# Kernel optimization log

Measured on AMD Instinct MI355X. Metric: run time of the kernel, lower is better.

The kernel has to match this reference:

```python
import jax, jax.numpy as jnp
import numpy as np

B, L, D, Y = 8, 2500, 512, 8921

def setup_inputs() -> dict:
    key = jax.random.key(0)
    k1, k2, k3, k4 = jax.random.split(key, 4)
    x = jax.random.normal(k1, (B, L, D), dtype=jnp.float32)
    # xavier-ish init scale for the label-attention and output matrices
    scale = (2.0 / (Y + D)) ** 0.5
    U_w = jax.random.normal(k2, (Y, D), dtype=jnp.float32) * scale
    final_w = jax.random.normal(k3, (Y, D), dtype=jnp.float32) * scale
    final_b = jax.random.normal(k4, (Y,), dtype=jnp.float32) * 0.01
    return {"x": x, "U_w": U_w, "final_w": final_w, "final_b": final_b}

def reference(x, U_w, final_w, final_b):
    # scores[b, y, l] = U_w[y, :] . x[b, l, :]
    scores = jnp.einsum('yd,bld->byl', U_w, x)            # (B, Y, L)
    alpha = jax.nn.softmax(scores, axis=2)                 # softmax over seq dim
    m = jnp.einsum('byl,bld->byd', alpha, x)               # (B, Y, D)
    y = jnp.einsum('yd,byd->by', final_w, m) + final_b     # (B, Y)
    return y
```

## Files before the change

kernel.cpp:

```cpp
#include <hip/hip_runtime.h>
#include <hip/hip_bf16.h>

#define NB 8
#define NL 2500
#define ND 512
#define NY 8921

#define BM 256
#define BN 256
#define BK 32
#define NKS 16
#define LPAD 2560
#define NLT 10
#define NYB 70
#define YPAD 8960

#define SPLIT 5
#define LSPL_MAIN 2

#define TILE 16384
#define GT_BYTES ((size_t)NYB * NKS * TILE)
#define XT_BYTES ((size_t)NB * NLT * NKS * TILE)
#define P_ELEMS  ((size_t)SPLIT * NB * YPAD)
#define P_BYTES  (P_ELEMS * 4)

typedef short s8v __attribute__((ext_vector_type(8)));
typedef float f4v __attribute__((ext_vector_type(4)));

__device__ __forceinline__ unsigned short f2bf(float f) {
  unsigned int u = __float_as_uint(f);
  return (unsigned short)((u + 0x7FFFu + ((u >> 16) & 1u)) >> 16);
}
__device__ __forceinline__ unsigned int pk2(float a, float b) {
  return (unsigned int)f2bf(a) | ((unsigned int)f2bf(b) << 16);
}
__device__ __forceinline__ void async_copy16(const char* g, char* l) {
  __builtin_amdgcn_global_load_lds(
      (const __attribute__((address_space(1))) void*)g,
      (__attribute__((address_space(3))) void*)l, 16, 0, 0);
}

__device__ __forceinline__ int tile_off(int r, int gn) {
  int rp = r >> 1;
  return rp * 128 + ((((r & 1) << 6) | (gn << 4)) ^ ((rp & 7) << 4));
}

__global__ void cvt_g_kernel(const float* __restrict__ U, const float* __restrict__ W,
                             char* __restrict__ Gt) {
  int c = blockIdx.x * 256 + threadIdx.x;
  int g10 = c & 1023;
  int tile = c >> 10;
  int ks = tile & 15, yblk = tile >> 4;
  int r = g10 >> 2, gn = g10 & 3;
  int rg = yblk * 256 + r;
  int y = rg >> 1;
  uint4 o;
  if (y < NY) {
    const float* src = (rg & 1) ? W : U;
    const float4* p = (const float4*)(src + (size_t)y * ND + ks * BK + gn * 8);
    float4 f0 = p[0], f1 = p[1];
    o.x = pk2(f0.x, f0.y); o.y = pk2(f0.z, f0.w);
    o.z = pk2(f1.x, f1.y); o.w = pk2(f1.z, f1.w);
  } else {
    o = make_uint4(0u, 0u, 0u, 0u);
  }
  *(uint4*)(Gt + (size_t)tile * TILE + tile_off(r, gn)) = o;
}

__global__ void cvt_x_kernel(const float* __restrict__ x, char* __restrict__ Xt) {
  int c = blockIdx.x * 256 + threadIdx.x;
  int g10 = c & 1023;
  int tile = c >> 10;
  int ks = tile & 15, rest = tile >> 4;
  int t = rest % NLT, b = rest / NLT;
  int r = g10 >> 2, gn = g10 & 3;
  int l = t * 256 + r;
  uint4 o;
  if (l < NL) {
    const float4* p = (const float4*)(x + ((size_t)b * NL + l) * ND + ks * BK + gn * 8);
    float4 f0 = p[0], f1 = p[1];
    o.x = pk2(f0.x, f0.y); o.y = pk2(f0.z, f0.w);
    o.z = pk2(f1.x, f1.y); o.w = pk2(f1.z, f1.w);
  } else {
    o = make_uint4(0u, 0u, 0u, 0u);
  }
  *(uint4*)(Xt + (size_t)tile * TILE + tile_off(r, gn)) = o;
}

template<int LSPL, int NSPL, bool PARTIAL>
__global__ __launch_bounds__(512, 2) void fused_kernel(
    const char* __restrict__ Gt, const char* __restrict__ Xt,
    const float* __restrict__ bias, float* __restrict__ out,
    float* __restrict__ PD, float* __restrict__ PN)
{
  __shared__ uint4 ring[8192];
  char* ringC = (char*)ring;

  constexpr int NKT = LSPL * 8;

  const int tid  = threadIdx.x;
  const int lane = tid & 63;
  const int w    = tid >> 6;
  const int wr   = w >> 2;
  const int wc   = w & 3;
  const int cl   = lane & 15, g = lane >> 4;

  const int id    = blockIdx.x;
  const int bb    = id & 7;
  const int n     = id >> 3;
  const int yblk  = n / NSPL;
  const int split = n - yblk * NSPL;
  const int tbase = split * LSPL;

  const char* GA = Gt + (size_t)yblk * NKS * TILE;
  const char* XB = Xt + ((size_t)bb * NLT + tbase) * NKS * TILE;

  f4v acc[8][4];
  float runD[8][2], runN[8][2];
  #pragma unroll
  for (int mi = 0; mi < 8; ++mi)
    #pragma unroll
    for (int p = 0; p < 2; ++p) { runD[mi][p] = 0.f; runN[mi][p] = 0.f; }

  int aoff[8], boff[4];
  #pragma unroll
  for (int j = 0; j < 8; ++j) aoff[j] = tile_off(wr * 128 + j * 16 + cl, g);
  #pragma unroll
  for (int ni = 0; ni < 4; ++ni) boff[ni] = tile_off(wc * 64 + ni * 16 + cl, g);

  const int t16 = tid << 4;
  auto stgA = [&](int kt1, int par) {
    const char* ga = GA + (size_t)((((kt1 & 7) << 1) | par)) * TILE;
    char* la = ringC + (kt1 & 1) * 32768 + par * 16384 + (w << 10);
    async_copy16(ga + t16, la);
    async_copy16(ga + 8192 + t16, la + 8192);
  };
  auto stgB = [&](int kt1, int par) {
    const char* gb = XB + (size_t)((kt1 >> 3) * 16 + ((kt1 & 7) << 1) + par) * TILE;
    char* lb = ringC + 65536 + (kt1 & 1) * 32768 + par * 16384 + (w << 10);
    async_copy16(gb + t16, lb);
    async_copy16(gb + 8192 + t16, lb + 8192);
  };

  auto softmax_acc = [&](int tt) {
    const int lbase = (tbase + tt) * BN + wc * 64 + cl;
    #pragma unroll
    for (int mi = 0; mi < 8; ++mi) {
      #pragma unroll
      for (int p = 0; p < 2; ++p) {
        float se = 0.f, ste = 0.f;
        #pragma unroll
        for (int ni = 0; ni < 4; ++ni) {
          bool valid = (lbase + ni * 16) < NL;
          float sv = valid ? acc[mi][ni][2 * p] : -1e30f;
          float e = __expf(sv);
          se += e;
          ste += e * acc[mi][ni][2 * p + 1];
        }
        runD[mi][p] += se;
        runN[mi][p] += ste;
      }
    }
  };

#define SBAR __builtin_amdgcn_sched_barrier(0)
#define LGKM(N) asm volatile("s_waitcnt lgkmcnt(" #N ")" ::: "memory")
#define VMC(N)  asm volatile("s_waitcnt vmcnt(" #N ")" ::: "memory")

  stgA(0, 0); stgB(0, 0); stgA(0, 1); stgB(0, 1);
  VMC(4);
  __builtin_amdgcn_s_barrier();
  asm volatile("" ::: "memory");

  s8v bvE[4], bvO[4], afX[4], afY[4];
  #pragma unroll
  for (int ni = 0; ni < 4; ++ni) bvE[ni] = *(const s8v*)(ringC + 65536 + boff[ni]);
  #pragma unroll
  for (int j = 0; j < 4; ++j)    afX[j] = *(const s8v*)(ringC + aoff[j]);

  for (int kt = 0; kt < NKT; ++kt) {
    const int buf = kt & 1;
    const char* Ae = ringC + buf * 32768;
    const char* Ao = Ae + 16384;
    const char* Bo = ringC + 65536 + buf * 32768 + 16384;
    const char* Aen = ringC + (buf ^ 1) * 32768;
    const char* Ben = ringC + 65536 + (buf ^ 1) * 32768;
    const bool hn = (kt + 1) < NKT;

    if ((kt & 7) == 0) {
      if (kt > 0) softmax_acc((kt >> 3) - 1);
      #pragma unroll
      for (int mi = 0; mi < 8; ++mi)
        #pragma unroll
        for (int ni = 0; ni < 4; ++ni)
          #pragma unroll
          for (int q = 0; q < 4; ++q) acc[mi][ni][q] = 0.f;
    }

    if (hn) stgA(kt + 1, 0);
    #pragma unroll
    for (int j = 0; j < 4; ++j) afY[j] = *(const s8v*)(Ae + aoff[4 + j]);
    SBAR;
    __builtin_amdgcn_s_barrier();
    LGKM(4); SBAR;
    __builtin_amdgcn_s_setprio(1);
    #pragma unroll
    for (int j = 0; j < 4; ++j)
      #pragma unroll
      for (int ni = 0; ni < 4; ++ni)
        acc[j][ni] = __builtin_amdgcn_mfma_f32_16x16x32_bf16(afX[j], bvE[ni], acc[j][ni], 0, 0, 0);
    __builtin_amdgcn_s_setprio(0);
    if (hn) { VMC(2); } else { VMC(0); }
    SBAR;
    __builtin_amdgcn_s_barrier();
    asm volatile("" ::: "memory");

    if (hn) stgB(kt + 1, 0);
    #pragma unroll
    for (int ni = 0; ni < 4; ++ni) bvO[ni] = *(const s8v*)(Bo + boff[ni]);
    #pragma unroll
    for (int j = 0; j < 4; ++j)    afX[j] = *(const s8v*)(Ao + aoff[j]);
    SBAR;
    __builtin_amdgcn_s_barrier();
    LGKM(8); SBAR;
    __builtin_amdgcn_s_setprio(1);
    #pragma unroll
    for (int j = 0; j < 4; ++j)
      #pragma unroll
      for (int ni = 0; ni < 4; ++ni)
        acc[4 + j][ni] = __builtin_amdgcn_mfma_f32_16x16x32_bf16(afY[j], bvE[ni], acc[4 + j][ni], 0, 0, 0);
    __builtin_amdgcn_s_setprio(0);
    SBAR;
    __builtin_amdgcn_s_barrier();
    asm volatile("" ::: "memory");

    if (hn) stgA(kt + 1, 1);
    #pragma unroll
    for (int j = 0; j < 4; ++j) afY[j] = *(const s8v*)(Ao + aoff[4 + j]);
    SBAR;
    __builtin_amdgcn_s_barrier();
    LGKM(4); SBAR;
    __builtin_amdgcn_s_setprio(1);
    #pragma unroll
    for (int j = 0; j < 4; ++j)
      #pragma unroll
      for (int ni = 0; ni < 4; ++ni)
        acc[j][ni] = __builtin_amdgcn_mfma_f32_16x16x32_bf16(afX[j], bvO[ni], acc[j][ni], 0, 0, 0);
    __builtin_amdgcn_s_setprio(0);
    if (hn) VMC(2);
    SBAR;
    __builtin_amdgcn_s_barrier();
    asm volatile("" ::: "memory");

    if (hn) {
      stgB(kt + 1, 1);
      #pragma unroll
      for (int ni = 0; ni < 4; ++ni) bvE[ni] = *(const s8v*)(Ben + boff[ni]);
      #pragma unroll
      for (int j = 0; j < 4; ++j)    afX[j] = *(const s8v*)(Aen + aoff[j]);
      SBAR;
      __builtin_amdgcn_s_barrier();
      LGKM(8); SBAR;
    } else {
      SBAR;
      __builtin_amdgcn_s_barrier();
      LGKM(0); SBAR;
    }
    __builtin_amdgcn_s_setprio(1);
    #pragma unroll
    for (int j = 0; j < 4; ++j)
      #pragma unroll
      for (int ni = 0; ni < 4; ++ni)
        acc[4 + j][ni] = __builtin_amdgcn_mfma_f32_16x16x32_bf16(afY[j], bvO[ni], acc[4 + j][ni], 0, 0, 0);
    __builtin_amdgcn_s_setprio(0);
    SBAR;
    __builtin_amdgcn_s_barrier();
    asm volatile("" ::: "memory");
  }
  softmax_acc(LSPL - 1);

#undef SBAR
#undef LGKM
#undef VMC

  #pragma unroll
  for (int mi = 0; mi < 8; ++mi)
    #pragma unroll
    for (int p = 0; p < 2; ++p) {
      float d = runD[mi][p], nn = runN[mi][p];
      #pragma unroll
      for (int off = 1; off < 16; off <<= 1) {
        d += __shfl_xor(d, off);
        nn += __shfl_xor(nn, off);
      }
      runD[mi][p] = d; runN[mi][p] = nn;
    }

  __syncthreads();
  float* sm = (float*)ring;
  if (cl == 0) {
    #pragma unroll
    for (int mi = 0; mi < 8; ++mi)
      #pragma unroll
      for (int p = 0; p < 2; ++p) {
        int lab = wr * 64 + mi * 8 + 2 * g + p;
        float* s2 = sm + (lab * 4 + wc) * 2;
        s2[0] = runD[mi][p]; s2[1] = runN[mi][p];
      }
  }
  __syncthreads();
  if (tid < 128) {
    float D = 0.f, N = 0.f;
    #pragma unroll
    for (int q = 0; q < 4; ++q) {
      const float* s2 = sm + (tid * 4 + q) * 2;
      D += s2[0]; N += s2[1];
    }
    int y = yblk * 128 + tid;
    if constexpr (PARTIAL) {
      size_t o = ((size_t)split * NB + bb) * YPAD + y;
      PD[o] = D; PN[o] = N;
    } else {
      if (y < NY) out[(size_t)bb * NY + y] = N / D + bias[y];
    }
  }
}

__global__ void merge_kernel(const float* __restrict__ PD, const float* __restrict__ PN,
                             const float* __restrict__ bias, float* __restrict__ out) {
  int idx = blockIdx.x * 256 + threadIdx.x;
  int b = idx / YPAD, y = idx - b * YPAD;
  if (y >= NY) return;
  float D = 0.f, N = 0.f;
  #pragma unroll
  for (int s = 0; s < SPLIT; ++s) {
    size_t o = ((size_t)s * NB + b) * YPAD + y;
    D += PD[o];
    N += PN[o];
  }
  out[(size_t)b * NY + y] = N / D + bias[y];
}

extern "C" void kernel_launch(void* const* d_in, const int* in_sizes, int n_in,
                              void* d_out, int out_size, void* d_ws, size_t ws_size,
                              hipStream_t stream) {
  const float* xf   = (const float*)d_in[0];
  const float* Uf   = (const float*)d_in[1];
  const float* Wf   = (const float*)d_in[2];
  const float* bias = (const float*)d_in[3];
  float* out = (float*)d_out;

  char* Gt = (char*)d_ws;
  char* Xt = Gt + GT_BYTES;
  float* PD = (float*)(Xt + XT_BYTES);
  float* PN = PD + P_ELEMS;

  cvt_g_kernel<<<4480, 256, 0, stream>>>(Uf, Wf, Gt);
  cvt_x_kernel<<<5120, 256, 0, stream>>>(xf, Xt);

  const size_t need_main = GT_BYTES + XT_BYTES + 2 * P_BYTES;
  if (ws_size >= need_main) {
    fused_kernel<LSPL_MAIN, SPLIT, true><<<NYB * NB * SPLIT, 512, 0, stream>>>(
        Gt, Xt, bias, out, PD, PN);
    merge_kernel<<<NB * YPAD / 256, 256, 0, stream>>>(PD, PN, bias, out);
  } else {
    fused_kernel<NLT, 1, false><<<NYB * NB, 512, 0, stream>>>(
        Gt, Xt, bias, out, PD, PN);
  }
}
```

Measured before the change: 361.6 us.

## Switch GEMM from 16x16x32 to 32x32x16 MFMA with new warp tiling

Replaces the 16x16x32 bf16 MFMA with the larger 32x32x16 instruction and remaps the 8 waves from a 2x4 to a 4x2 grid, each computing 64x128 instead of 128x64. Fragment loads, LDS offsets, the softmax accumulation, the cross-lane reductions and the label index mapping are all rewritten for the 32x32 accumulator layout. The aim is to cut LDS fragment traffic per MFMA and raise per-instruction throughput. In exchange the output-row mapping becomes more intricate, which risks correctness errors, and the LDS read pattern changes, which may add bank conflicts.

```diff
diff --git a/kernel.cpp b/kernel.cpp
--- a/kernel.cpp
+++ b/kernel.cpp
@@ -24,8 +24,8 @@
 #define P_ELEMS  ((size_t)SPLIT * NB * YPAD)
 #define P_BYTES  (P_ELEMS * 4)
 
-typedef short s8v __attribute__((ext_vector_type(8)));
-typedef float f4v __attribute__((ext_vector_type(4)));
+typedef short s8v  __attribute__((ext_vector_type(8)));
+typedef float f16v __attribute__((ext_vector_type(16)));
 
 __device__ __forceinline__ unsigned short f2bf(float f) {
   unsigned int u = __float_as_uint(f);
@@ -101,9 +101,10 @@
   const int tid  = threadIdx.x;
   const int lane = tid & 63;
   const int w    = tid >> 6;
-  const int wr   = w >> 2;
-  const int wc   = w & 3;
-  const int cl   = lane & 15, g = lane >> 4;
+  const int wrm  = w >> 1;
+  const int wcn  = w & 1;
+  const int c32  = lane & 31;
+  const int hi   = lane >> 5;
 
   const int id    = blockIdx.x;
   const int bb    = id & 7;
@@ -115,18 +116,26 @@
   const char* GA = Gt + (size_t)yblk * NKS * TILE;
   const char* XB = Xt + ((size_t)bb * NLT + tbase) * NKS * TILE;
 
-  f4v acc[8][4];
-  float runD[8][2], runN[8][2];
-  #pragma unroll
-  for (int mi = 0; mi < 8; ++mi)
-    #pragma unroll
-    for (int p = 0; p < 2; ++p) { runD[mi][p] = 0.f; runN[mi][p] = 0.f; }
-
-  int aoff[8], boff[4];
-  #pragma unroll
-  for (int j = 0; j < 8; ++j) aoff[j] = tile_off(wr * 128 + j * 16 + cl, g);
-  #pragma unroll
-  for (int ni = 0; ni < 4; ++ni) boff[ni] = tile_off(wc * 64 + ni * 16 + cl, g);
+  f16v acc[2][4];
+  float runD[2][8], runN[2][8];
+  #pragma unroll
+  for (int mi = 0; mi < 2; ++mi)
+    #pragma unroll
+    for (int j = 0; j < 8; ++j) { runD[mi][j] = 0.f; runN[mi][j] = 0.f; }
+
+  int aoffE[2], aoffO[2], boffE[4], boffO[4];
+  #pragma unroll
+  for (int mi = 0; mi < 2; ++mi) {
+    int r = wrm * 64 + mi * 32 + c32;
+    aoffE[mi] = tile_off(r, hi);
+    aoffO[mi] = tile_off(r, 2 + hi);
+  }
+  #pragma unroll
+  for (int ni = 0; ni < 4; ++ni) {
+    int r = wcn * 128 + ni * 32 + c32;
+    boffE[ni] = tile_off(r, hi);
+    boffO[ni] = tile_off(r, 2 + hi);
+  }
 
   const int t16 = tid << 4;
   auto stgA = [&](int kt1, int par) {
@@ -143,22 +152,22 @@
   };
 
   auto softmax_acc = [&](int tt) {
-    const int lbase = (tbase + tt) * BN + wc * 64 + cl;
-    #pragma unroll
-    for (int mi = 0; mi < 8; ++mi) {
-      #pragma unroll
-      for (int p = 0; p < 2; ++p) {
+    const int lb0 = (tbase + tt) * BN + wcn * 128 + c32;
+    #pragma unroll
+    for (int mi = 0; mi < 2; ++mi) {
+      #pragma unroll
+      for (int j = 0; j < 8; ++j) {
         float se = 0.f, ste = 0.f;
         #pragma unroll
         for (int ni = 0; ni < 4; ++ni) {
-          bool valid = (lbase + ni * 16) < NL;
-          float sv = valid ? acc[mi][ni][2 * p] : -1e30f;
+          bool valid = (lb0 + ni * 32) < NL;
+          float sv = valid ? acc[mi][ni][2 * j] : -1e30f;
           float e = __expf(sv);
           se += e;
-          ste += e * acc[mi][ni][2 * p + 1];
+          ste += e * acc[mi][ni][2 * j + 1];
         }
-        runD[mi][p] += se;
-        runN[mi][p] += ste;
+        runD[mi][j] += se;
+        runN[mi][j] += ste;
       }
     }
   };
@@ -172,43 +181,46 @@
   __builtin_amdgcn_s_barrier();
   asm volatile("" ::: "memory");
 
-  s8v bvE[4], bvO[4], afX[4], afY[4];
-  #pragma unroll
-  for (int ni = 0; ni < 4; ++ni) bvE[ni] = *(const s8v*)(ringC + 65536 + boff[ni]);
-  #pragma unroll
-  for (int j = 0; j < 4; ++j)    afX[j] = *(const s8v*)(ringC + aoff[j]);
+  s8v afX[2], bvX[4], afY[2], bvY[4];
+  #pragma unroll
+  for (int mi = 0; mi < 2; ++mi) afX[mi] = *(const s8v*)(ringC + aoffE[mi]);
+  #pragma unroll
+  for (int ni = 0; ni < 4; ++ni) bvX[ni] = *(const s8v*)(ringC + 65536 + boffE[ni]);
 
   for (int kt = 0; kt < NKT; ++kt) {
     const int buf = kt & 1;
-    const char* Ae = ringC + buf * 32768;
-    const char* Ao = Ae + 16384;
-    const char* Bo = ringC + 65536 + buf * 32768 + 16384;
-    const char* Aen = ringC + (buf ^ 1) * 32768;
-    const char* Ben = ringC + 65536 + (buf ^ 1) * 32768;
+    const char* A0 = ringC + buf * 32768;
+    const char* A1 = A0 + 16384;
+    const char* B0 = ringC + 65536 + buf * 32768;
+    const char* B1 = B0 + 16384;
+    const char* A0n = ringC + (buf ^ 1) * 32768;
+    const char* B0n = ringC + 65536 + (buf ^ 1) * 32768;
     const bool hn = (kt + 1) < NKT;
 
     if ((kt & 7) == 0) {
       if (kt > 0) softmax_acc((kt >> 3) - 1);
       #pragma unroll
-      for (int mi = 0; mi < 8; ++mi)
+      for (int mi = 0; mi < 2; ++mi)
         #pragma unroll
         for (int ni = 0; ni < 4; ++ni)
           #pragma unroll
-          for (int q = 0; q < 4; ++q) acc[mi][ni][q] = 0.f;
+          for (int q = 0; q < 16; ++q) acc[mi][ni][q] = 0.f;
     }
 
     if (hn) stgA(kt + 1, 0);
     #pragma unroll
-    for (int j = 0; j < 4; ++j) afY[j] = *(const s8v*)(Ae + aoff[4 + j]);
-    SBAR;
-    __builtin_amdgcn_s_barrier();
-    LGKM(4); SBAR;
+    for (int mi = 0; mi < 2; ++mi) afY[mi] = *(const s8v*)(A0 + aoffO[mi]);
+    #pragma unroll
+    for (int ni = 0; ni < 4; ++ni) bvY[ni] = *(const s8v*)(B0 + boffO[ni]);
+    SBAR;
+    __builtin_amdgcn_s_barrier();
+    LGKM(6); SBAR;
     __builtin_amdgcn_s_setprio(1);
     #pragma unroll
-    for (int j = 0; j < 4; ++j)
+    for (int mi = 0; mi < 2; ++mi)
       #pragma unroll
       for (int ni = 0; ni < 4; ++ni)
-        acc[j][ni] = __builtin_amdgcn_mfma_f32_16x16x32_bf16(afX[j], bvE[ni], acc[j][ni], 0, 0, 0);
+        acc[mi][ni] = __builtin_amdgcn_mfma_f32_32x32x16_bf16(afX[mi], bvX[ni], acc[mi][ni], 0, 0, 0);
     __builtin_amdgcn_s_setprio(0);
     if (hn) { VMC(2); } else { VMC(0); }
     SBAR;
@@ -217,18 +229,18 @@
 
     if (hn) stgB(kt + 1, 0);
     #pragma unroll
-    for (int ni = 0; ni < 4; ++ni) bvO[ni] = *(const s8v*)(Bo + boff[ni]);
-    #pragma unroll
-    for (int j = 0; j < 4; ++j)    afX[j] = *(const s8v*)(Ao + aoff[j]);
-    SBAR;
-    __builtin_amdgcn_s_barrier();
-    LGKM(8); SBAR;
+    for (int mi = 0; mi < 2; ++mi) afX[mi] = *(const s8v*)(A1 + aoffE[mi]);
+    #pragma unroll
+    for (int ni = 0; ni < 4; ++ni) bvX[ni] = *(const s8v*)(B1 + boffE[ni]);
+    SBAR;
+    __builtin_amdgcn_s_barrier();
+    LGKM(6); SBAR;
     __builtin_amdgcn_s_setprio(1);
     #pragma unroll
-    for (int j = 0; j < 4; ++j)
+    for (int mi = 0; mi < 2; ++mi)
       #pragma unroll
       for (int ni = 0; ni < 4; ++ni)
-        acc[4 + j][ni] = __builtin_amdgcn_mfma_f32_16x16x32_bf16(afY[j], bvE[ni], acc[4 + j][ni], 0, 0, 0);
+        acc[mi][ni] = __builtin_amdgcn_mfma_f32_32x32x16_bf16(afY[mi], bvY[ni], acc[mi][ni], 0, 0, 0);
     __builtin_amdgcn_s_setprio(0);
     SBAR;
     __builtin_amdgcn_s_barrier();
@@ -236,16 +248,18 @@
 
     if (hn) stgA(kt + 1, 1);
     #pragma unroll
-    for (int j = 0; j < 4; ++j) afY[j] = *(const s8v*)(Ao + aoff[4 + j]);
-    SBAR;
-    __builtin_amdgcn_s_barrier();
-    LGKM(4); SBAR;
+    for (int mi = 0; mi < 2; ++mi) afY[mi] = *(const s8v*)(A1 + aoffO[mi]);
+    #pragma unroll
+    for (int ni = 0; ni < 4; ++ni) bvY[ni] = *(const s8v*)(B1 + boffO[ni]);
+    SBAR;
+    __builtin_amdgcn_s_barrier();
+    LGKM(6); SBAR;
     __builtin_amdgcn_s_setprio(1);
     #pragma unroll
-    for (int j = 0; j < 4; ++j)
+    for (int mi = 0; mi < 2; ++mi)
       #pragma unroll
       for (int ni = 0; ni < 4; ++ni)
-        acc[j][ni] = __builtin_amdgcn_mfma_f32_16x16x32_bf16(afX[j], bvO[ni], acc[j][ni], 0, 0, 0);
+        acc[mi][ni] = __builtin_amdgcn_mfma_f32_32x32x16_bf16(afX[mi], bvX[ni], acc[mi][ni], 0, 0, 0);
     __builtin_amdgcn_s_setprio(0);
     if (hn) VMC(2);
     SBAR;
@@ -255,12 +269,12 @@
     if (hn) {
       stgB(kt + 1, 1);
       #pragma unroll
-      for (int ni = 0; ni < 4; ++ni) bvE[ni] = *(const s8v*)(Ben + boff[ni]);
-      #pragma unroll
-      for (int j = 0; j < 4; ++j)    afX[j] = *(const s8v*)(Aen + aoff[j]);
+      for (int mi = 0; mi < 2; ++mi) afX[mi] = *(const s8v*)(A0n + aoffE[mi]);
+      #pragma unroll
+      for (int ni = 0; ni < 4; ++ni) bvX[ni] = *(const s8v*)(B0n + boffE[ni]);
       SBAR;
       __builtin_amdgcn_s_barrier();
-      LGKM(8); SBAR;
+      LGKM(6); SBAR;
     } else {
       SBAR;
       __builtin_amdgcn_s_barrier();
@@ -268,10 +282,10 @@
     }
     __builtin_amdgcn_s_setprio(1);
     #pragma unroll
-    for (int j = 0; j < 4; ++j)
+    for (int mi = 0; mi < 2; ++mi)
       #pragma unroll
       for (int ni = 0; ni < 4; ++ni)
-        acc[4 + j][ni] = __builtin_amdgcn_mfma_f32_16x16x32_bf16(afY[j], bvO[ni], acc[4 + j][ni], 0, 0, 0);
+        acc[mi][ni] = __builtin_amdgcn_mfma_f32_32x32x16_bf16(afY[mi], bvY[ni], acc[mi][ni], 0, 0, 0);
     __builtin_amdgcn_s_setprio(0);
     SBAR;
     __builtin_amdgcn_s_barrier();
@@ -284,36 +298,37 @@
 #undef VMC
 
   #pragma unroll
-  for (int mi = 0; mi < 8; ++mi)
-    #pragma unroll
-    for (int p = 0; p < 2; ++p) {
-      float d = runD[mi][p], nn = runN[mi][p];
-      #pragma unroll
-      for (int off = 1; off < 16; off <<= 1) {
+  for (int mi = 0; mi < 2; ++mi)
+    #pragma unroll
+    for (int j = 0; j < 8; ++j) {
+      float d = runD[mi][j], nn = runN[mi][j];
+      #pragma unroll
+      for (int off = 1; off < 32; off <<= 1) {
         d += __shfl_xor(d, off);
         nn += __shfl_xor(nn, off);
       }
-      runD[mi][p] = d; runN[mi][p] = nn;
-    }
-
+      runD[mi][j] = d; runN[mi][j] = nn;
+    }
+
+  const int jl[8] = {0, 1, 4, 5, 8, 9, 12, 13};
   __syncthreads();
   float* sm = (float*)ring;
-  if (cl == 0) {
-    #pragma unroll
-    for (int mi = 0; mi < 8; ++mi)
-      #pragma unroll
-      for (int p = 0; p < 2; ++p) {
-        int lab = wr * 64 + mi * 8 + 2 * g + p;
-        float* s2 = sm + (lab * 4 + wc) * 2;
-        s2[0] = runD[mi][p]; s2[1] = runN[mi][p];
+  if (c32 == 0) {
+    #pragma unroll
+    for (int mi = 0; mi < 2; ++mi)
+      #pragma unroll
+      for (int j = 0; j < 8; ++j) {
+        int lab = wrm * 32 + mi * 16 + jl[j] + 2 * hi;
+        float* s2 = sm + (lab * 2 + wcn) * 2;
+        s2[0] = runD[mi][j]; s2[1] = runN[mi][j];
       }
   }
   __syncthreads();
   if (tid < 128) {
     float D = 0.f, N = 0.f;
     #pragma unroll
-    for (int q = 0; q < 4; ++q) {
-      const float* s2 = sm + (tid * 4 + q) * 2;
+    for (int q = 0; q < 2; ++q) {
+      const float* s2 = sm + (tid * 2 + q) * 2;
       D += s2[0]; N += s2[1];
     }
     int y = yblk * 128 + tid;
```

Measured after the change: 409.0 us. 1.13x slower.
